# Kernel optimization log

Hardware: AMD Instinct MI355X
Metric: run time of the kernel (lower is better)

## Reference

```python
import jax, jax.numpy as jnp
import numpy as np

B, H, L, D = 1, 8, 2048, 64
DP = 3   # positional coord dim
RE = 1   # extra relative features appended via concat
F = DP + RE  # LazyLinear in-features


def setup_inputs() -> dict:
    key = jax.random.key(0)
    ks = jax.random.split(key, 12)
    return {
        "q": jax.random.normal(ks[0], (B, H, L, D), jnp.float32),
        "k": jax.random.normal(ks[1], (B, H, L, D), jnp.float32),
        "v": jax.random.normal(ks[2], (B, H, L, D), jnp.float32),
        "c": jax.random.uniform(ks[3], (B, 1, 1, L), jnp.float32),
        "d_q": jax.random.normal(ks[4], (B, L, DP), jnp.float32),
        "d_k_top": jax.random.normal(ks[5], (B, L, DP), jnp.float32),
        "d_k_bot": jax.random.normal(ks[6], (B, L, DP), jnp.float32),
        "d_k_score": jax.random.uniform(ks[7], (B, L, 2, F), jnp.float32),
        "relative_top": jax.random.normal(ks[8], (B, L, L, RE), jnp.float32),
        "relative_bottom": jax.random.normal(ks[9], (B, L, L, RE), jnp.float32),
        "W_w": jax.random.normal(ks[10], (F, H), jnp.float32) * 0.1,
        "W_b": jax.random.normal(ks[11], (F, H), jnp.float32) * 0.1,
    }


def _pairwise_diff(a, b):
    # a: [B,Lq,Dp], b: [B,Lk,Dp] -> [B,Lq,Lk,Dp]
    return a[:, :, None, :] - b[:, None, :, :]


def reference(q, k, v, c, d_q, d_k_top, d_k_bot, d_k_score,
              relative_top, relative_bottom, W_w, W_b):
    # score function: scaled dot product -> [B,H,Lq,Lk]
    scores = jnp.einsum('bhqd,bhkd->bhqk', q, k) * (q.shape[-1] ** -0.5)

    # relative-position bias path
    dt = jnp.concatenate([_pairwise_diff(d_q, d_k_top), relative_top], axis=-1)     # [B,Lq,Lk,F]
    db = jnp.concatenate([_pairwise_diff(d_q, d_k_bot), relative_bottom], axis=-1)  # [B,Lq,Lk,F]
    dm = jnp.stack([dt, db], axis=3)                 # [B,Lq,Lk,2,F]
    dm = dm * d_k_score[:, None]                     # broadcast over Lq
    dm = dm.sum(axis=3)                              # [B,Lq,Lk,F]

    w = jax.nn.softplus(dm @ W_w).transpose(0, 3, 1, 2)  # [B,H,Lq,Lk]
    b = (dm @ W_b).transpose(0, 3, 1, 2)                 # [B,H,Lq,Lk]
    scores = scores * w + b

    # leaky probability function: softmax gated by per-key sampling weights c
    probs = jax.nn.softmax(scores, axis=-1) * c      # [B,H,Lq,Lk]

    out = jnp.einsum('bhqk,bhkd->bhqd', probs, v)
    return out, probs
```

## Files before the change

### kernel.cpp

```cpp
#include <hip/hip_runtime.h>
#include <cstdint>
#include <cstddef>

#define NH 8
#define LQ 2048
#define DH 64
#define NKT_HALF 16

typedef __attribute__((ext_vector_type(8))) __bf16 bf16x8;
typedef __attribute__((ext_vector_type(8))) unsigned short ushort8;
typedef __attribute__((ext_vector_type(4))) float floatx4;

__device__ __forceinline__ unsigned short bf_trunc(float x) {
    return (unsigned short)(__float_as_uint(x) >> 16);
}
__device__ __forceinline__ float bf_up(unsigned short h) {
    return __uint_as_float(((unsigned int)h) << 16);
}
__device__ __forceinline__ unsigned short bf_rne(float x) {
    unsigned int u = __float_as_uint(x);
    return (unsigned short)((u + 0x7FFFu + ((u >> 16) & 1u)) >> 16);
}
struct hl_t { unsigned short h, l; };
__device__ __forceinline__ hl_t split2(float x) {
    hl_t r;
    r.h = bf_trunc(x);
    r.l = bf_trunc(x - bf_up(r.h));
    return r;
}

#define MFMA16(A, B, C) __builtin_amdgcn_mfma_f32_16x16x32_bf16((A), (B), (C), 0, 0, 0)

__global__ __launch_bounds__(256, 3) void attn_main(
    const float* __restrict__ qp,  const float* __restrict__ kp,
    const float* __restrict__ vp,  const float* __restrict__ cp,
    const float* __restrict__ dqp, const float* __restrict__ dktp,
    const float* __restrict__ dkbp,const float* __restrict__ dksp,
    const float* __restrict__ rtp, const float* __restrict__ rbp,
    const float* __restrict__ Wwp, const float* __restrict__ Wbp,
    float* __restrict__ probp, float* __restrict__ lws, float* __restrict__ pvws)
{
    __shared__ unsigned short sh_khi[64 * 72];
    __shared__ unsigned short sh_klo[64 * 72];
    __shared__ unsigned short sh_vhi[64 * 72];
    __shared__ unsigned short sh_vlo[64 * 72];
    __shared__ float sh_meta[64 * 13];
    __shared__ float sh_dqs[64 * 3];

    const int bid  = blockIdx.x;
    const int half = bid & 1;
    const int h    = (bid >> 1) & 7;
    const int qt   = bid >> 4;
    const int q0   = qt * 64;
    const int t    = threadIdx.x;
    const int lane = t & 63;
    const int m    = lane & 15;
    const int quad = lane >> 4;
    const int w16  = (t >> 6) * 16;

    float Ww[4], Wb[4];
#pragma unroll
    for (int f = 0; f < 4; ++f) { Ww[f] = Wwp[f * NH + h]; Wb[f] = Wbp[f * NH + h]; }

    {
        const int row = t >> 2, s = t & 3;
        const float* src = qp + ((size_t)(h * LQ + q0 + row)) * DH + s * 16;
        ushort8 vh0, vh1, vl0, vl1;
#pragma unroll
        for (int j = 0; j < 2; ++j) {
            float4 x = *(const float4*)(src + 4 * j);
            hl_t a = split2(x.x), b = split2(x.y), c = split2(x.z), d = split2(x.w);
            vh0[4 * j + 0] = a.h; vl0[4 * j + 0] = a.l;
            vh0[4 * j + 1] = b.h; vl0[4 * j + 1] = b.l;
            vh0[4 * j + 2] = c.h; vl0[4 * j + 2] = c.l;
            vh0[4 * j + 3] = d.h; vl0[4 * j + 3] = d.l;
        }
#pragma unroll
        for (int j = 0; j < 2; ++j) {
            float4 x = *(const float4*)(src + 8 + 4 * j);
            hl_t a = split2(x.x), b = split2(x.y), c = split2(x.z), d = split2(x.w);
            vh1[4 * j + 0] = a.h; vl1[4 * j + 0] = a.l;
            vh1[4 * j + 1] = b.h; vl1[4 * j + 1] = b.l;
            vh1[4 * j + 2] = c.h; vl1[4 * j + 2] = c.l;
            vh1[4 * j + 3] = d.h; vl1[4 * j + 3] = d.l;
        }
        const int base = row * 72 + s * 16;
        *(ushort8*)&sh_khi[base] = vh0;  *(ushort8*)&sh_khi[base + 8] = vh1;
        *(ushort8*)&sh_klo[base] = vl0;  *(ushort8*)&sh_klo[base + 8] = vl1;
        if (t < 64) {
            sh_dqs[t * 3 + 0] = dqp[(q0 + t) * 3 + 0];
            sh_dqs[t * 3 + 1] = dqp[(q0 + t) * 3 + 1];
            sh_dqs[t * 3 + 2] = dqp[(q0 + t) * 3 + 2];
        }
    }
    __syncthreads();

    bf16x8 aqh[2], aql[2];
#pragma unroll
    for (int kc = 0; kc < 2; ++kc) {
        aqh[kc] = *(const bf16x8*)&sh_khi[(w16 + m) * 72 + kc * 32 + quad * 8];
        aql[kc] = *(const bf16x8*)&sh_klo[(w16 + m) * 72 + kc * 32 + quad * 8];
    }
    float dq0[4], dq1[4], dq2[4];
#pragma unroll
    for (int r = 0; r < 4; ++r) {
        const int row = w16 + quad * 4 + r;
        dq0[r] = sh_dqs[row * 3 + 0]; dq1[r] = sh_dqs[row * 3 + 1]; dq2[r] = sh_dqs[row * 3 + 2];
    }
    __syncthreads();

    const floatx4 zf = {0.f, 0.f, 0.f, 0.f};
    floatx4 pacc[4] = {zf, zf, zf, zf};
    float lpart[4] = {0.f, 0.f, 0.f, 0.f};

    for (int kth = 0; kth < NKT_HALF; ++kth) {
        const int k0 = (half * NKT_HALF + kth) * 64;

        {
            const int row = t >> 2, s = t & 3;
            const float* src = kp + ((size_t)(h * LQ + k0 + row)) * DH + s * 16;
            ushort8 vh0, vh1, vl0, vl1;
#pragma unroll
            for (int j = 0; j < 2; ++j) {
                float4 x = *(const float4*)(src + 4 * j);
                hl_t a = split2(x.x), b = split2(x.y), c = split2(x.z), d = split2(x.w);
                vh0[4 * j + 0] = a.h; vl0[4 * j + 0] = a.l;
                vh0[4 * j + 1] = b.h; vl0[4 * j + 1] = b.l;
                vh0[4 * j + 2] = c.h; vl0[4 * j + 2] = c.l;
                vh0[4 * j + 3] = d.h; vl0[4 * j + 3] = d.l;
            }
#pragma unroll
            for (int j = 0; j < 2; ++j) {
                float4 x = *(const float4*)(src + 8 + 4 * j);
                hl_t a = split2(x.x), b = split2(x.y), c = split2(x.z), d = split2(x.w);
                vh1[4 * j + 0] = a.h; vl1[4 * j + 0] = a.l;
                vh1[4 * j + 1] = b.h; vl1[4 * j + 1] = b.l;
                vh1[4 * j + 2] = c.h; vl1[4 * j + 2] = c.l;
                vh1[4 * j + 3] = d.h; vl1[4 * j + 3] = d.l;
            }
            const int base = row * 72 + s * 16;
            *(ushort8*)&sh_khi[base] = vh0;  *(ushort8*)&sh_khi[base + 8] = vh1;
            *(ushort8*)&sh_klo[base] = vl0;  *(ushort8*)&sh_klo[base + 8] = vl1;
        }
        {
            const int p = t >> 4;
            const int mm = t & 15;
#pragma unroll
            for (int g = 0; g < 2; ++g) {
                const int kka = 2 * p + 32 * g;
                const float ca = cp[k0 + kka], cb = cp[k0 + kka + 1];
                const float* va = vp + ((size_t)(h * LQ + k0 + kka)) * DH;
                const float* vb = va + DH;
#pragma unroll
                for (int dd = 0; dd < 4; ++dd) {
                    const int d = mm + 16 * dd;
                    hl_t xa = split2(va[d] * ca);
                    hl_t xb = split2(vb[d] * cb);
                    *(unsigned int*)&sh_vhi[d * 72 + kka] = (unsigned int)xa.h | ((unsigned int)xb.h << 16);
                    *(unsigned int*)&sh_vlo[d * 72 + kka] = (unsigned int)xa.l | ((unsigned int)xb.l << 16);
                }
            }
        }
        if (t < 64) {
            const int kg = k0 + t;
            const float* sc_ = dksp + (size_t)kg * 8;
            const float* tp  = dktp + (size_t)kg * 3;
            const float* bt  = dkbp + (size_t)kg * 3;
            float cw = 0.f, cb2 = 0.f;
#pragma unroll
            for (int f = 0; f < 3; ++f) {
                const float stf = sc_[f], sbf = sc_[4 + f];
                const float A  = stf + sbf;
                const float Bv = tp[f] * stf + bt[f] * sbf;
                sh_meta[t * 13 + f]     = A * Ww[f];
                sh_meta[t * 13 + 4 + f] = A * Wb[f];
                cw  -= Bv * Ww[f];
                cb2 -= Bv * Wb[f];
            }
            sh_meta[t * 13 + 3]  = cw;              sh_meta[t * 13 + 7]  = cb2;
            sh_meta[t * 13 + 8]  = sc_[3] * Ww[3];  sh_meta[t * 13 + 9]  = sc_[7] * Ww[3];
            sh_meta[t * 13 + 10] = sc_[3] * Wb[3];  sh_meta[t * 13 + 11] = sc_[7] * Wb[3];
        }
        __syncthreads();

        float rt_[4][4], rb_[4][4];
#pragma unroll
        for (int r = 0; r < 4; ++r) {
            const size_t q = (size_t)(q0 + w16 + quad * 4 + r);
#pragma unroll
            for (int nt = 0; nt < 4; ++nt) {
                rt_[nt][r] = rtp[q * LQ + k0 + nt * 16 + m];
                rb_[nt][r] = rbp[q * LQ + k0 + nt * 16 + m];
            }
        }

        floatx4 sc[4] = {zf, zf, zf, zf};
#pragma unroll
        for (int nt = 0; nt < 4; ++nt) {
#pragma unroll
            for (int kc = 0; kc < 2; ++kc) {
                const int kb = (nt * 16 + m) * 72 + kc * 32 + quad * 8;
                bf16x8 bh = *(const bf16x8*)&sh_khi[kb];
                bf16x8 bl = *(const bf16x8*)&sh_klo[kb];
                sc[nt] = MFMA16(aqh[kc], bh, sc[nt]);
                sc[nt] = MFMA16(aql[kc], bh, sc[nt]);
                sc[nt] = MFMA16(aqh[kc], bl, sc[nt]);
            }
        }
        __syncthreads();

        unsigned short* ebf = sh_klo;
#pragma unroll
        for (int nt = 0; nt < 4; ++nt) {
            const int kcol = nt * 16 + m;
            const float m0 = sh_meta[kcol * 13 + 0],  m1 = sh_meta[kcol * 13 + 1];
            const float m2 = sh_meta[kcol * 13 + 2],  m3 = sh_meta[kcol * 13 + 3];
            const float m4 = sh_meta[kcol * 13 + 4],  m5 = sh_meta[kcol * 13 + 5];
            const float m6 = sh_meta[kcol * 13 + 6],  m7 = sh_meta[kcol * 13 + 7];
            const float m8 = sh_meta[kcol * 13 + 8],  m9 = sh_meta[kcol * 13 + 9];
            const float mA = sh_meta[kcol * 13 + 10], mB = sh_meta[kcol * 13 + 11];
#pragma unroll
            for (int r = 0; r < 4; ++r) {
                float ww = fmaf(dq0[r], m0, m3); ww = fmaf(dq1[r], m1, ww); ww = fmaf(dq2[r], m2, ww);
                ww = fmaf(rt_[nt][r], m8, ww);   ww = fmaf(rb_[nt][r], m9, ww);
                float bb = fmaf(dq0[r], m4, m7); bb = fmaf(dq1[r], m5, bb); bb = fmaf(dq2[r], m6, bb);
                bb = fmaf(rt_[nt][r], mA, bb);   bb = fmaf(rb_[nt][r], mB, bb);
                const float wg = fmaxf(ww, 0.f) + __logf(1.f + __expf(-fabsf(ww)));
                const float sv = fmaf(sc[nt][r] * 0.125f, wg, bb);
                const float e  = __expf(sv - 8.0f);
                lpart[r] += e;
                probp[((size_t)(h * LQ + q0 + w16 + quad * 4 + r)) * LQ + k0 + kcol] = e;
                ebf[(w16 + quad * 4 + r) * 72 + kcol] = bf_rne(e);
            }
        }

        bf16x8 ap0 = *(const bf16x8*)&ebf[(w16 + m) * 72 + quad * 8];
        bf16x8 ap1 = *(const bf16x8*)&ebf[(w16 + m) * 72 + 32 + quad * 8];
#pragma unroll
        for (int nt = 0; nt < 4; ++nt) {
            const int vb = (nt * 16 + m) * 72 + quad * 8;
            bf16x8 bh0 = *(const bf16x8*)&sh_vhi[vb];
            bf16x8 bl0 = *(const bf16x8*)&sh_vlo[vb];
            bf16x8 bh1 = *(const bf16x8*)&sh_vhi[vb + 32];
            bf16x8 bl1 = *(const bf16x8*)&sh_vlo[vb + 32];
            pacc[nt] = MFMA16(ap0, bh0, pacc[nt]);
            pacc[nt] = MFMA16(ap0, bl0, pacc[nt]);
            pacc[nt] = MFMA16(ap1, bh1, pacc[nt]);
            pacc[nt] = MFMA16(ap1, bl1, pacc[nt]);
        }
        __syncthreads();
    }

#pragma unroll
    for (int off = 1; off < 16; off <<= 1) {
#pragma unroll
        for (int r = 0; r < 4; ++r) lpart[r] += __shfl_xor(lpart[r], off, 64);
    }
    if (m == 0) {
#pragma unroll
        for (int r = 0; r < 4; ++r)
            lws[half * (NH * LQ) + h * LQ + q0 + w16 + quad * 4 + r] = lpart[r];
    }
#pragma unroll
    for (int nt = 0; nt < 4; ++nt) {
#pragma unroll
        for (int r = 0; r < 4; ++r) {
            const size_t row = (size_t)(h * LQ + q0 + w16 + quad * 4 + r);
            pvws[(size_t)half * (NH * LQ * DH) + row * DH + nt * 16 + m] = pacc[nt][r];
        }
    }
}

__global__ void combine_kernel(const float* __restrict__ pvws, const float* __restrict__ lws,
                               float* __restrict__ outp)
{
    const int idx4 = blockIdx.x * 256 + threadIdx.x;
    const int row  = idx4 >> 4;
    const int d4   = (idx4 & 15) * 4;
    const float4 a = *(const float4*)(pvws + (size_t)row * DH + d4);
    const float4 b = *(const float4*)(pvws + (size_t)(NH * LQ * DH) + (size_t)row * DH + d4);
    const float rl = 1.0f / (lws[row] + lws[NH * LQ + row]);
    *(float4*)(outp + (size_t)row * DH + d4) =
        make_float4((a.x + b.x) * rl, (a.y + b.y) * rl, (a.z + b.z) * rl, (a.w + b.w) * rl);
}

__global__ void norm_kernel(float* __restrict__ probp, const float* __restrict__ cp,
                            const float* __restrict__ lws)
{
    const int row = blockIdx.x;
    const float rl = 1.0f / (lws[row] + lws[NH * LQ + row]);
    float* p = probp + (size_t)row * LQ;
    const int t = threadIdx.x;
    float4 x0 = *(const float4*)(p + t * 4);
    float4 x1 = *(const float4*)(p + (t + 256) * 4);
    const float4 c0 = *(const float4*)(cp + t * 4);
    const float4 c1 = *(const float4*)(cp + (t + 256) * 4);
    x0.x *= rl * c0.x; x0.y *= rl * c0.y; x0.z *= rl * c0.z; x0.w *= rl * c0.w;
    x1.x *= rl * c1.x; x1.y *= rl * c1.y; x1.z *= rl * c1.z; x1.w *= rl * c1.w;
    *(float4*)(p + t * 4)         = x0;
    *(float4*)(p + (t + 256) * 4) = x1;
}

extern "C" void kernel_launch(void* const* d_in, const int* in_sizes, int n_in,
                              void* d_out, int out_size, void* d_ws, size_t ws_size,
                              hipStream_t stream)
{
    (void)in_sizes; (void)n_in; (void)ws_size; (void)out_size;
    const float* qp   = (const float*)d_in[0];
    const float* kp   = (const float*)d_in[1];
    const float* vp   = (const float*)d_in[2];
    const float* cp   = (const float*)d_in[3];
    const float* dqp  = (const float*)d_in[4];
    const float* dktp = (const float*)d_in[5];
    const float* dkbp = (const float*)d_in[6];
    const float* dksp = (const float*)d_in[7];
    const float* rtp  = (const float*)d_in[8];
    const float* rbp  = (const float*)d_in[9];
    const float* Wwp  = (const float*)d_in[10];
    const float* Wbp  = (const float*)d_in[11];

    float* outp  = (float*)d_out;
    float* probp = (float*)d_out + (size_t)NH * LQ * DH;

    float* lws  = (float*)d_ws;
    float* pvws = (float*)d_ws + 2 * (NH * LQ);

    attn_main<<<dim3(512), dim3(256), 0, stream>>>(
        qp, kp, vp, cp, dqp, dktp, dkbp, dksp, rtp, rbp, Wwp, Wbp, probp, lws, pvws);
    combine_kernel<<<dim3(1024), dim3(256), 0, stream>>>(pvws, lws, outp);
    norm_kernel<<<dim3(NH * LQ), dim3(256), 0, stream>>>(probp, cp, lws);
}
```

Before: 292.9 us.

## Split keys four ways, fold scale into Q, use exp2, batch norm rows

```diff
diff --git a/kernel.cpp b/kernel.cpp
--- a/kernel.cpp
+++ b/kernel.cpp
@@ -5,7 +5,7 @@
 #define NH 8
 #define LQ 2048
 #define DH 64
-#define NKT_HALF 16
+#define NKT_Q 8
 
 typedef __attribute__((ext_vector_type(8))) __bf16 bf16x8;
 typedef __attribute__((ext_vector_type(8))) unsigned short ushort8;
@@ -31,7 +31,7 @@
 
 #define MFMA16(A, B, C) __builtin_amdgcn_mfma_f32_16x16x32_bf16((A), (B), (C), 0, 0, 0)
 
-__global__ __launch_bounds__(256, 3) void attn_main(
+__global__ __launch_bounds__(256, 4) void attn_main(
     const float* __restrict__ qp,  const float* __restrict__ kp,
     const float* __restrict__ vp,  const float* __restrict__ cp,
     const float* __restrict__ dqp, const float* __restrict__ dktp,
@@ -48,9 +48,9 @@
     __shared__ float sh_dqs[64 * 3];
 
     const int bid  = blockIdx.x;
-    const int half = bid & 1;
-    const int h    = (bid >> 1) & 7;
-    const int qt   = bid >> 4;
+    const int quar = bid & 3;
+    const int h    = (bid >> 2) & 7;
+    const int qt   = bid >> 5;
     const int q0   = qt * 64;
     const int t    = threadIdx.x;
     const int lane = t & 63;
@@ -69,7 +69,8 @@
 #pragma unroll
         for (int j = 0; j < 2; ++j) {
             float4 x = *(const float4*)(src + 4 * j);
-            hl_t a = split2(x.x), b = split2(x.y), c = split2(x.z), d = split2(x.w);
+            hl_t a = split2(x.x * 0.125f), b = split2(x.y * 0.125f);
+            hl_t c = split2(x.z * 0.125f), d = split2(x.w * 0.125f);
             vh0[4 * j + 0] = a.h; vl0[4 * j + 0] = a.l;
             vh0[4 * j + 1] = b.h; vl0[4 * j + 1] = b.l;
             vh0[4 * j + 2] = c.h; vl0[4 * j + 2] = c.l;
@@ -78,7 +79,8 @@
 #pragma unroll
         for (int j = 0; j < 2; ++j) {
             float4 x = *(const float4*)(src + 8 + 4 * j);
-            hl_t a = split2(x.x), b = split2(x.y), c = split2(x.z), d = split2(x.w);
+            hl_t a = split2(x.x * 0.125f), b = split2(x.y * 0.125f);
+            hl_t c = split2(x.z * 0.125f), d = split2(x.w * 0.125f);
             vh1[4 * j + 0] = a.h; vl1[4 * j + 0] = a.l;
             vh1[4 * j + 1] = b.h; vl1[4 * j + 1] = b.l;
             vh1[4 * j + 2] = c.h; vl1[4 * j + 2] = c.l;
@@ -113,8 +115,8 @@
     floatx4 pacc[4] = {zf, zf, zf, zf};
     float lpart[4] = {0.f, 0.f, 0.f, 0.f};
 
-    for (int kth = 0; kth < NKT_HALF; ++kth) {
-        const int k0 = (half * NKT_HALF + kth) * 64;
+    for (int kth = 0; kth < NKT_Q; ++kth) {
+        const int k0 = (quar * NKT_Q + kth) * 64;
 
         {
             const int row = t >> 2, s = t & 3;
@@ -225,9 +227,9 @@
                 ww = fmaf(rt_[nt][r], m8, ww);   ww = fmaf(rb_[nt][r], m9, ww);
                 float bb = fmaf(dq0[r], m4, m7); bb = fmaf(dq1[r], m5, bb); bb = fmaf(dq2[r], m6, bb);
                 bb = fmaf(rt_[nt][r], mA, bb);   bb = fmaf(rb_[nt][r], mB, bb);
-                const float wg = fmaxf(ww, 0.f) + __logf(1.f + __expf(-fabsf(ww)));
-                const float sv = fmaf(sc[nt][r] * 0.125f, wg, bb);
-                const float e  = __expf(sv - 8.0f);
+                const float wg = __logf(1.0f + __builtin_amdgcn_exp2f(ww * 1.44269504f));
+                const float sv = fmaf(sc[nt][r], wg, bb);
+                const float e  = __builtin_amdgcn_exp2f(fmaf(sv, 1.44269504f, -11.5415603f));
                 lpart[r] += e;
                 probp[((size_t)(h * LQ + q0 + w16 + quad * 4 + r)) * LQ + k0 + kcol] = e;
                 ebf[(w16 + quad * 4 + r) * 72 + kcol] = bf_rne(e);
@@ -259,14 +261,14 @@
     if (m == 0) {
 #pragma unroll
         for (int r = 0; r < 4; ++r)
-            lws[half * (NH * LQ) + h * LQ + q0 + w16 + quad * 4 + r] = lpart[r];
+            lws[quar * (NH * LQ) + h * LQ + q0 + w16 + quad * 4 + r] = lpart[r];
     }
 #pragma unroll
     for (int nt = 0; nt < 4; ++nt) {
 #pragma unroll
         for (int r = 0; r < 4; ++r) {
             const size_t row = (size_t)(h * LQ + q0 + w16 + quad * 4 + r);
-            pvws[(size_t)half * (NH * LQ * DH) + row * DH + nt * 16 + m] = pacc[nt][r];
+            pvws[(size_t)quar * (NH * LQ * DH) + row * DH + nt * 16 + m] = pacc[nt][r];
         }
     }
 }
@@ -277,28 +279,41 @@
     const int idx4 = blockIdx.x * 256 + threadIdx.x;
     const int row  = idx4 >> 4;
     const int d4   = (idx4 & 15) * 4;
-    const float4 a = *(const float4*)(pvws + (size_t)row * DH + d4);
-    const float4 b = *(const float4*)(pvws + (size_t)(NH * LQ * DH) + (size_t)row * DH + d4);
-    const float rl = 1.0f / (lws[row] + lws[NH * LQ + row]);
-    *(float4*)(outp + (size_t)row * DH + d4) =
-        make_float4((a.x + b.x) * rl, (a.y + b.y) * rl, (a.z + b.z) * rl, (a.w + b.w) * rl);
-}
-
-__global__ void norm_kernel(float* __restrict__ probp, const float* __restrict__ cp,
-                            const float* __restrict__ lws)
+    const size_t stride = (size_t)NH * LQ * DH;
+    floatx4 s = {0.f, 0.f, 0.f, 0.f};
+    float l = 0.f;
+#pragma unroll
+    for (int qr = 0; qr < 4; ++qr) {
+        s += *(const floatx4*)(pvws + qr * stride + (size_t)row * DH + d4);
+        l += lws[qr * (NH * LQ) + row];
+    }
+    const float rl = 1.0f / l;
+    *(floatx4*)(outp + (size_t)row * DH + d4) = s * rl;
+}
+
+__global__ __launch_bounds__(256) void norm_kernel(float* __restrict__ probp,
+                                                   const float* __restrict__ cp,
+                                                   const float* __restrict__ lws)
 {
-    const int row = blockIdx.x;
-    const float rl = 1.0f / (lws[row] + lws[NH * LQ + row]);
-    float* p = probp + (size_t)row * LQ;
-    const int t = threadIdx.x;
-    float4 x0 = *(const float4*)(p + t * 4);
-    float4 x1 = *(const float4*)(p + (t + 256) * 4);
-    const float4 c0 = *(const float4*)(cp + t * 4);
-    const float4 c1 = *(const float4*)(cp + (t + 256) * 4);
-    x0.x *= rl * c0.x; x0.y *= rl * c0.y; x0.z *= rl * c0.z; x0.w *= rl * c0.w;
-    x1.x *= rl * c1.x; x1.y *= rl * c1.y; x1.z *= rl * c1.z; x1.w *= rl * c1.w;
-    *(float4*)(p + t * 4)         = x0;
-    *(float4*)(p + (t + 256) * 4) = x1;
+    const int r0 = blockIdx.x * 4;
+    const int t  = threadIdx.x;
+    const floatx4 c0 = *(const floatx4*)(cp + t * 4);
+    const floatx4 c1 = *(const floatx4*)(cp + (t + 256) * 4);
+#pragma unroll
+    for (int r = 0; r < 4; ++r) {
+        const int row = r0 + r;
+        float l = 0.f;
+#pragma unroll
+        for (int qr = 0; qr < 4; ++qr) l += lws[qr * (NH * LQ) + row];
+        const float rl = 1.0f / l;
+        float* p = probp + (size_t)row * LQ;
+        floatx4 x0 = *(const floatx4*)(p + t * 4);
+        floatx4 x1 = *(const floatx4*)(p + (t + 256) * 4);
+        x0 = x0 * c0 * rl;
+        x1 = x1 * c1 * rl;
+        __builtin_nontemporal_store(x0, (floatx4*)(p + t * 4));
+        __builtin_nontemporal_store(x1, (floatx4*)(p + (t + 256) * 4));
+    }
 }
 
 extern "C" void kernel_launch(void* const* d_in, const int* in_sizes, int n_in,
@@ -323,10 +338,10 @@
     float* probp = (float*)d_out + (size_t)NH * LQ * DH;
 
     float* lws  = (float*)d_ws;
-    float* pvws = (float*)d_ws + 2 * (NH * LQ);
-
-    attn_main<<<dim3(512), dim3(256), 0, stream>>>(
+    float* pvws = (float*)d_ws + 4 * (NH * LQ);
+
+    attn_main<<<dim3(1024), dim3(256), 0, stream>>>(
         qp, kp, vp, cp, dqp, dktp, dkbp, dksp, rtp, rbp, Wwp, Wbp, probp, lws, pvws);
     combine_kernel<<<dim3(1024), dim3(256), 0, stream>>>(pvws, lws, outp);
-    norm_kernel<<<dim3(NH * LQ), dim3(256), 0, stream>>>(probp, cp, lws);
-}
+    norm_kernel<<<dim3(4096), dim3(256), 0, stream>>>(probp, cp, lws);
+}
```

After: 329.0 us. 1.12x slower.
